# Kernel optimization log

Measured on AMD Instinct MI355X. Metric: run time of the kernel, lower is better.

Reference implementation:

```python
import jax, jax.numpy as jnp
import numpy as np
import math

B, N, D, H, FFN = 4, 2048, 512, 8, 2048
DK = D // H
EPS = 1e-5


def _layer_norm(x, g, b):
    mu = jnp.mean(x, axis=-1, keepdims=True)
    var = jnp.mean((x - mu) ** 2, axis=-1, keepdims=True)
    return (x - mu) * jax.lax.rsqrt(var + EPS) * g + b


def _rotate_half(x):
    h = x.shape[-1] // 2
    return jnp.concatenate([-x[..., h:], x[..., :h]], axis=-1)


def _rope(q, k, positions):
    # q, k: (B, H, N, DK); positions: (B, N) int
    inv_freq = 1.0 / (10000.0 ** (jnp.arange(0, DK, 2, dtype=jnp.float32) / DK))  # (DK/2,)
    ang = positions[:, None, :, None].astype(jnp.float32) * inv_freq  # (B,1,N,DK/2)
    cos = jnp.concatenate([jnp.cos(ang), jnp.cos(ang)], axis=-1)  # (B,1,N,DK)
    sin = jnp.concatenate([jnp.sin(ang), jnp.sin(ang)], axis=-1)
    q = q * cos + _rotate_half(q) * sin
    k = k * cos + _rotate_half(k) * sin
    return q, k


def setup_inputs() -> dict:
    key = jax.random.key(0)
    ks = jax.random.split(key, 16)
    s = 0.02
    x = jax.random.normal(ks[0], (B, N, D), dtype=jnp.float32)
    # backward-looking hop mask within jobs: random boolean with True diagonal
    m = jax.random.uniform(ks[1], (B, N, N)) < 0.1
    o2o_mask = m | jnp.eye(N, dtype=bool)[None]
    positions = jax.random.randint(ks[2], (B, N), 0, N)
    params = {
        'wq': jax.random.normal(ks[3], (D, D)) * s, 'bq': jnp.zeros((D,)),
        'wk': jax.random.normal(ks[4], (D, D)) * s, 'bk': jnp.zeros((D,)),
        'wv': jax.random.normal(ks[5], (D, D)) * s, 'bv': jnp.zeros((D,)),
        'wo': jax.random.normal(ks[6], (D, D)) * s, 'bo': jnp.zeros((D,)),
        'ln1_g': jnp.ones((D,)), 'ln1_b': jnp.zeros((D,)),
        'ln2_g': jnp.ones((D,)), 'ln2_b': jnp.zeros((D,)),
        'w1': jax.random.normal(ks[7], (D, FFN)) * s, 'b1': jnp.zeros((FFN,)),
        'w2': jax.random.normal(ks[8], (FFN, D)) * s, 'b2': jnp.zeros((D,)),
    }
    return {'x': x, 'o2o_mask': o2o_mask, 'positions': positions, **params}


def reference(x, o2o_mask, positions, wq, bq, wk, bk, wv, bv, wo, bo,
              ln1_g, ln1_b, ln2_g, ln2_b, w1, b1, w2, b2):
    residual = x
    xn = _layer_norm(x, ln1_g, ln1_b)
    q = (xn @ wq + bq).reshape(B, N, H, DK).transpose(0, 2, 1, 3)
    k = (xn @ wk + bk).reshape(B, N, H, DK).transpose(0, 2, 1, 3)
    v = (xn @ wv + bv).reshape(B, N, H, DK).transpose(0, 2, 1, 3)
    q, k = _rope(q, k, positions)
    scores = jnp.einsum('bhqd,bhkd->bhqk', q, k) / math.sqrt(DK)
    scores = jnp.where(o2o_mask[:, None], scores, -jnp.inf)
    attn = jax.nn.softmax(scores, axis=-1)
    attn = jnp.where(jnp.isnan(attn), 0.0, attn)  # fully-masked rows -> 0
    attn_out = jnp.einsum('bhqk,bhkd->bhqd', attn, v)
    attn_out = attn_out.transpose(0, 2, 1, 3).reshape(B, N, D)
    x = residual + (attn_out @ wo + bo)
    residual = x
    h = _layer_norm(x, ln2_g, ln2_b)
    h = jax.nn.relu(h @ w1 + b1) @ w2 + b2
    return residual + h
```

## Files before the change

kernel.cpp:

```cpp
#include <hip/hip_runtime.h>
#include <hip/hip_bf16.h>
#include <math.h>

typedef __attribute__((ext_vector_type(8))) __bf16 bf16x8;
typedef __attribute__((ext_vector_type(4))) __bf16 bf16x4;
typedef __attribute__((ext_vector_type(4))) float f32x4;

#define B_ 4
#define N_ 2048
#define D_ 512
#define H_ 8
#define DK_ 64
#define F_ 2048

__device__ __forceinline__ void async16(const __bf16* g, __bf16* l) {
  __builtin_amdgcn_global_load_lds((const __attribute__((address_space(1))) void*)g,
                                   (__attribute__((address_space(3))) void*)l, 16, 0, 0);
}

__global__ __launch_bounds__(256) void prep_all(const float* __restrict__ wq,
                                                const float* __restrict__ wk,
                                                const float* __restrict__ wv,
                                                const float* __restrict__ wo,
                                                const float* __restrict__ w1,
                                                const float* __restrict__ w2,
                                                const float* __restrict__ bq,
                                                const float* __restrict__ bk,
                                                const float* __restrict__ bv,
                                                __bf16* __restrict__ wqkvt,
                                                __bf16* __restrict__ wot,
                                                __bf16* __restrict__ w1t,
                                                __bf16* __restrict__ w2t,
                                                float* __restrict__ bqkv) {
  const int id = blockIdx.x;
  if (id >= 768) {
    int i = (id - 768) * 256 + threadIdx.x;
    bqkv[i] = (i < 512) ? bq[i] : (i < 1024) ? bk[i - 512] : bv[i - 1024];
    return;
  }
  __shared__ float t[64][65];
  const float* in;
  __bf16* outp;
  int k0, n0, K, Nc;
  if (id < 256) {
    const float* src[4] = {wq, wk, wv, wo};
    __bf16* dst[4] = {wqkvt, wqkvt + 512 * 512, wqkvt + 1024 * 512, wot};
    int w = id >> 6, tl = id & 63;
    in = src[w]; outp = dst[w]; k0 = (tl & 7) * 64; n0 = (tl >> 3) * 64; K = 512; Nc = 512;
  } else if (id < 512) {
    int tl = id - 256;
    in = w1; outp = w1t; k0 = (tl & 7) * 64; n0 = (tl >> 3) * 64; K = 512; Nc = 2048;
  } else {
    int tl = id - 512;
    in = w2; outp = w2t; k0 = (tl & 31) * 64; n0 = (tl >> 5) * 64; K = 2048; Nc = 512;
  }
  const int c = threadIdx.x & 63, r4 = threadIdx.x >> 6;
#pragma unroll
  for (int p = 0; p < 16; p++) {
    int rr = p * 4 + r4;
    t[rr][c] = in[(size_t)(k0 + rr) * Nc + n0 + c];
  }
  __syncthreads();
#pragma unroll
  for (int p = 0; p < 16; p++) {
    int rr = p * 4 + r4;
    outp[(size_t)(n0 + rr) * K + k0 + c] = (__bf16)t[c][rr];
  }
}

__global__ __launch_bounds__(256) void build_bitmask(const int* __restrict__ mask,
                                                     unsigned long long* __restrict__ bm) {
  size_t t = (size_t)blockIdx.x * 256 + threadIdx.x;
  int m = mask[t];
  unsigned long long w = __ballot(m != 0);
  if ((threadIdx.x & 63) == 0) bm[t >> 6] = w;
}

__global__ __launch_bounds__(256) void ln_fwd(const float* __restrict__ x,
                                              const float* __restrict__ g,
                                              const float* __restrict__ b,
                                              __bf16* __restrict__ out) {
  int row = blockIdx.x * 4 + (threadIdx.x >> 6);
  int lane = threadIdx.x & 63;
  const float* xr = x + (size_t)row * D_ + lane * 8;
  float4 a0 = *(const float4*)xr;
  float4 a1 = *(const float4*)(xr + 4);
  float v[8] = {a0.x, a0.y, a0.z, a0.w, a1.x, a1.y, a1.z, a1.w};
  float s = 0.f;
#pragma unroll
  for (int i = 0; i < 8; i++) s += v[i];
#pragma unroll
  for (int off = 1; off < 64; off <<= 1) s += __shfl_xor(s, off);
  float mu = s * (1.f / D_);
  float q = 0.f;
#pragma unroll
  for (int i = 0; i < 8; i++) { float d = v[i] - mu; q += d * d; }
#pragma unroll
  for (int off = 1; off < 64; off <<= 1) q += __shfl_xor(q, off);
  float rs = rsqrtf(q * (1.f / D_) + 1e-5f);
  const float* gp = g + lane * 8;
  const float* bp = b + lane * 8;
  alignas(16) __bf16 o[8];
#pragma unroll
  for (int i = 0; i < 8; i++) o[i] = (__bf16)((v[i] - mu) * rs * gp[i] + bp[i]);
  *(bf16x8*)(out + (size_t)row * D_ + lane * 8) = *(bf16x8*)o;
}

__global__ __launch_bounds__(256) void rope_vtrans(const __bf16* __restrict__ qkv,
                                                   const int* __restrict__ pos,
                                                   __bf16* __restrict__ qo,
                                                   __bf16* __restrict__ ko,
                                                   __bf16* __restrict__ vt) {
  __shared__ __bf16 tl[64][65];
  const int id = blockIdx.x;
  if (id < 8192) {
    int t = id * 256 + threadIdx.x;
    int d = t & 31;
    int h = (t >> 5) & 7;
    int n = (t >> 8) & (N_ - 1);
    int b = t >> 19;
    const __bf16* base = qkv + (size_t)(b * N_ + n) * 1536 + h * 64 + d;
    float q1 = (float)base[0], q2 = (float)base[32];
    float k1 = (float)base[512], k2 = (float)base[544];
    float p = (float)pos[b * N_ + n];
    float inv = __expf(-(float)d * (9.210340371976184f / 32.f));
    float ang = p * inv;
    float sn, cs;
    sincosf(ang, &sn, &cs);
    const float SC = 0.125f;
    size_t ob = ((size_t)(b * H_ + h) * N_ + n) * DK_ + d;
    qo[ob]      = (__bf16)((q1 * cs - q2 * sn) * SC);
    qo[ob + 32] = (__bf16)((q2 * cs + q1 * sn) * SC);
    ko[ob]      = (__bf16)(k1 * cs - k2 * sn);
    ko[ob + 32] = (__bf16)(k2 * cs + k1 * sn);
  } else {
    const int lin = id - 8192;
    const int n0 = (lin & 31) * 64, h = (lin >> 5) & 7, b = lin >> 8;
    const int c = threadIdx.x & 63, rr = threadIdx.x >> 6;
#pragma unroll
    for (int p = 0; p < 16; p++) {
      int i = p * 4 + rr;
      tl[i][c] = qkv[(size_t)(b * N_ + n0 + i) * 1536 + 1024 + h * 64 + c];
    }
    __syncthreads();
    size_t ob = (size_t)(b * H_ + h) * DK_ * N_;
#pragma unroll
    for (int p = 0; p < 16; p++) {
      int dd = p * 4 + rr;
      vt[ob + (size_t)dd * N_ + n0 + c] = tl[c][dd];
    }
  }
}

template <int RELU, int OBF, int RES>
__global__ __launch_bounds__(256) void gemm_bt(const __bf16* __restrict__ A,
                                               const __bf16* __restrict__ Bt,
                                               const float* __restrict__ bias,
                                               const float* __restrict__ res,
                                               void* __restrict__ Cout,
                                               int M, int N, int K) {
  __shared__ __bf16 As[2][128 * 32];
  __shared__ __bf16 Bs[2][128 * 32];
  const int tid = threadIdx.x;
  const int lane = tid & 63;
  const int wave = tid >> 6;
  const int quad = lane >> 4;
  const int l16 = lane & 15;
  const int m0 = blockIdx.y * 128;
  const int n0 = blockIdx.x * 128;
  const int wm = (wave >> 1) * 64;
  const int wn = (wave & 1) * 64;
  f32x4 acc[4][4] = {};

  const int c0 = tid, c1 = tid + 256;
  const int ar0 = c0 >> 2, ak0 = (c0 & 3) * 8;
  const int ar1 = c1 >> 2, ak1 = (c1 & 3) * 8;

  auto stage = [&](int k0, int buf) {
    async16(A + (size_t)(m0 + ar0) * K + k0 + ak0, As[buf] + c0 * 8);
    async16(A + (size_t)(m0 + ar1) * K + k0 + ak1, As[buf] + c1 * 8);
    async16(Bt + (size_t)(n0 + ar0) * K + k0 + ak0, Bs[buf] + c0 * 8);
    async16(Bt + (size_t)(n0 + ar1) * K + k0 + ak1, Bs[buf] + c1 * 8);
  };

  stage(0, 0);
  __syncthreads();
  const int niter = K >> 5;
  for (int it = 0; it < niter; it++) {
    const int buf = it & 1;
    if (it + 1 < niter) stage((it + 1) * 32, buf ^ 1);
    bf16x8 af[4], bf[4];
#pragma unroll
    for (int mi = 0; mi < 4; mi++)
      af[mi] = *(const bf16x8*)(As[buf] + (wm + mi * 16 + l16) * 32 + quad * 8);
#pragma unroll
    for (int ni = 0; ni < 4; ni++)
      bf[ni] = *(const bf16x8*)(Bs[buf] + (wn + ni * 16 + l16) * 32 + quad * 8);
#pragma unroll
    for (int mi = 0; mi < 4; mi++)
#pragma unroll
      for (int ni = 0; ni < 4; ni++)
        acc[mi][ni] = __builtin_amdgcn_mfma_f32_16x16x32_bf16(af[mi], bf[ni], acc[mi][ni], 0, 0, 0);
    __syncthreads();
  }
#pragma unroll
  for (int ni = 0; ni < 4; ni++) {
    const int col = n0 + wn + ni * 16 + l16;
    const float bv = bias[col];
#pragma unroll
    for (int mi = 0; mi < 4; mi++) {
#pragma unroll
      for (int r = 0; r < 4; r++) {
        const int row = m0 + wm + mi * 16 + quad * 4 + r;
        float v = acc[mi][ni][r] + bv;
        if (RES) v += res[(size_t)row * N + col];
        if (RELU) v = fmaxf(v, 0.f);
        if (OBF) ((__bf16*)Cout)[(size_t)row * N + col] = (__bf16)v;
        else     ((float*)Cout)[(size_t)row * N + col] = v;
      }
    }
  }
}

template <int RELU, int OBF, int RES>
__global__ __launch_bounds__(256) void gemm_bt64(const __bf16* __restrict__ A,
                                                 const __bf16* __restrict__ Bt,
                                                 const float* __restrict__ bias,
                                                 const float* __restrict__ res,
                                                 void* __restrict__ Cout,
                                                 int M, int N, int K) {
  __shared__ __bf16 As[2][128 * 32];
  __shared__ __bf16 Bs[2][64 * 32];
  const int tid = threadIdx.x;
  const int lane = tid & 63;
  const int wave = tid >> 6;
  const int quad = lane >> 4;
  const int l16 = lane & 15;
  const int m0 = blockIdx.y * 128;
  const int n0 = blockIdx.x * 64;
  const int wm = wave * 32;
  f32x4 acc[2][4] = {};

  const int ar0 = tid >> 2, ak0 = (tid & 3) * 8;

  auto stage = [&](int k0, int buf) {
    async16(A + (size_t)(m0 + ar0) * K + k0 + ak0, As[buf] + tid * 8);
    async16(A + (size_t)(m0 + 64 + ar0) * K + k0 + ak0, As[buf] + (tid + 256) * 8);
    async16(Bt + (size_t)(n0 + ar0) * K + k0 + ak0, Bs[buf] + tid * 8);
  };

  stage(0, 0);
  __syncthreads();
  const int niter = K >> 5;
  for (int it = 0; it < niter; it++) {
    const int buf = it & 1;
    if (it + 1 < niter) stage((it + 1) * 32, buf ^ 1);
    bf16x8 af[2], bf[4];
#pragma unroll
    for (int mi = 0; mi < 2; mi++)
      af[mi] = *(const bf16x8*)(As[buf] + (wm + mi * 16 + l16) * 32 + quad * 8);
#pragma unroll
    for (int ni = 0; ni < 4; ni++)
      bf[ni] = *(const bf16x8*)(Bs[buf] + (ni * 16 + l16) * 32 + quad * 8);
#pragma unroll
    for (int mi = 0; mi < 2; mi++)
#pragma unroll
      for (int ni = 0; ni < 4; ni++)
        acc[mi][ni] = __builtin_amdgcn_mfma_f32_16x16x32_bf16(af[mi], bf[ni], acc[mi][ni], 0, 0, 0);
    __syncthreads();
  }
#pragma unroll
  for (int ni = 0; ni < 4; ni++) {
    const int col = n0 + ni * 16 + l16;
    const float bv = bias[col];
#pragma unroll
    for (int mi = 0; mi < 2; mi++) {
#pragma unroll
      for (int r = 0; r < 4; r++) {
        const int row = m0 + wm + mi * 16 + quad * 4 + r;
        float v = acc[mi][ni][r] + bv;
        if (RES) v += res[(size_t)row * N + col];
        if (RELU) v = fmaxf(v, 0.f);
        if (OBF) ((__bf16*)Cout)[(size_t)row * N + col] = (__bf16)v;
        else     ((float*)Cout)[(size_t)row * N + col] = v;
      }
    }
  }
}

__global__ __launch_bounds__(512, 4) void flash_attn(const __bf16* __restrict__ q,
                                                     const __bf16* __restrict__ k,
                                                     const __bf16* __restrict__ vt,
                                                     const unsigned long long* __restrict__ bm,
                                                     __bf16* __restrict__ out) {
  const int bid = blockIdx.x;
  const int gl = ((bid & 7) << 6) | (bid >> 3);
  const int qt = gl & 15;
  const int h = (gl >> 4) & 7;
  const int b = gl >> 7;
  const int tid = threadIdx.x;
  const int lane = tid & 63, wave = tid >> 6;
  const int quad = lane >> 4, l16 = lane & 15;
  __shared__ __bf16 Ks[3][64 * 64];
  __shared__ __bf16 Vs[3][64 * 64];
  __shared__ __bf16 P[8][16 * 68];
  const size_t bh = (size_t)b * H_ + h;
  const __bf16* qp = q + (bh * N_ + qt * 128 + wave * 16) * DK_;
  bf16x8 qf[2];
#pragma unroll
  for (int ks = 0; ks < 2; ks++)
    qf[ks] = *(const bf16x8*)(qp + l16 * DK_ + ks * 32 + quad * 8);
  const __bf16* kbase = k + bh * N_ * DK_;
  const __bf16* vbase = vt + bh * DK_ * N_;
  const int qrow0 = qt * 128 + wave * 16 + l16;
  const unsigned long long* bmr = bm + (size_t)(b * N_ + qrow0) * (N_ / 64);
  const int xo = l16 & 7;

  f32x4 oacc[4] = {};
  float lsum = 0.f;

  const int sr = tid >> 3;
  const int sj = (tid & 7) ^ (sr & 7);
  const __bf16* ksrc = kbase + sr * DK_ + sj * 8;
  const __bf16* vsrc = vbase + (size_t)sr * N_ + sj * 8;

  auto stage = [&](int kt, int buf) {
    async16(ksrc + (size_t)kt * 64 * DK_, Ks[buf] + tid * 8);
    async16(vsrc + kt * 64, Vs[buf] + tid * 8);
  };

  stage(0, 0);
  stage(1, 1);
  unsigned long long mw = bmr[0];
  asm volatile("s_waitcnt vmcnt(3)" ::: "memory");
  __builtin_amdgcn_s_barrier();
  __builtin_amdgcn_sched_barrier(0);

  for (int kt = 0; kt < 32; kt++) {
    const int buf = kt % 3;
    const int nstage = (kt + 2 < 32) ? kt + 2 : 31;
    stage(nstage, (kt + 2) % 3);
    const int nmask = (kt + 1 < 32) ? kt + 1 : 31;
    const unsigned long long mw_nxt = bmr[nmask];

    const unsigned long long mws = mw >> (quad * 4);
#pragma unroll
    for (int ci = 0; ci < 4; ci++) {
      const int row = ci * 16 + l16;
      bf16x8 kf0 = *(const bf16x8*)(Ks[buf] + (row * 8 + (quad ^ xo)) * 8);
      bf16x8 kf1 = *(const bf16x8*)(Ks[buf] + (row * 8 + ((4 + quad) ^ xo)) * 8);
      f32x4 a = {0.f, 0.f, 0.f, 0.f};
      a = __builtin_amdgcn_mfma_f32_16x16x32_bf16(kf0, qf[0], a, 0, 0, 0);
      a = __builtin_amdgcn_mfma_f32_16x16x32_bf16(kf1, qf[1], a, 0, 0, 0);
      const unsigned int nib = (unsigned int)(mws >> (ci * 16)) & 15u;
      bf16x4 pk;
#pragma unroll
      for (int r4 = 0; r4 < 4; r4++) {
        float in = ((nib >> r4) & 1u) ? a[r4] : -1e30f;
        float p = __expf(in);
        lsum += p;
        pk[r4] = (__bf16)p;
      }
      *(bf16x4*)(&P[wave][0] + l16 * 68 + ci * 16 + quad * 4) = pk;
    }
    bf16x8 pf0 = *(const bf16x8*)(&P[wave][0] + l16 * 68 + quad * 8);
    bf16x8 pf1 = *(const bf16x8*)(&P[wave][0] + l16 * 68 + 32 + quad * 8);
#pragma unroll
    for (int ni = 0; ni < 4; ni++) {
      const int row = ni * 16 + l16;
      bf16x8 vf0 = *(const bf16x8*)(Vs[buf] + (row * 8 + (quad ^ xo)) * 8);
      bf16x8 vf1 = *(const bf16x8*)(Vs[buf] + (row * 8 + ((4 + quad) ^ xo)) * 8);
      oacc[ni] = __builtin_amdgcn_mfma_f32_16x16x32_bf16(vf0, pf0, oacc[ni], 0, 0, 0);
      oacc[ni] = __builtin_amdgcn_mfma_f32_16x16x32_bf16(vf1, pf1, oacc[ni], 0, 0, 0);
    }
    asm volatile("s_waitcnt vmcnt(3)" ::: "memory");
    __builtin_amdgcn_s_barrier();
    __builtin_amdgcn_sched_barrier(0);
    mw = mw_nxt;
  }
  lsum += __shfl_xor(lsum, 16);
  lsum += __shfl_xor(lsum, 32);
  const float inv_l = (lsum > 0.f) ? 1.f / lsum : 0.f;
#pragma unroll
  for (int ni = 0; ni < 4; ni++) {
    bf16x4 ov;
#pragma unroll
    for (int r = 0; r < 4; r++) ov[r] = (__bf16)(oacc[ni][r] * inv_l);
    *(bf16x4*)(out + ((size_t)b * N_ + qrow0) * D_ + h * DK_ + ni * 16 + quad * 4) = ov;
  }
}

static constexpr size_t OFF_XN  = 0;
static constexpr size_t OFF_WT  = 8388608;
static constexpr size_t OFF_WO  = OFF_WT + 1572864;
static constexpr size_t OFF_W1  = OFF_WO + 524288;
static constexpr size_t OFF_W2  = OFF_W1 + 2097152;
static constexpr size_t OFF_BQ  = OFF_W2 + 2097152;
static constexpr size_t OFF_QKV = OFF_BQ + 6144;
static constexpr size_t OFF_QR  = OFF_QKV + 25165824;
static constexpr size_t OFF_KR  = OFF_QR + 8388608;
static constexpr size_t OFF_VT  = OFF_KR + 8388608;
static constexpr size_t OFF_AO  = OFF_VT + 8388608;
static constexpr size_t OFF_Y   = OFF_AO + 8388608;

extern "C" void kernel_launch(void* const* d_in, const int* in_sizes, int n_in,
                              void* d_out, int out_size, void* d_ws, size_t ws_size,
                              hipStream_t stream) {
  const float* x    = (const float*)d_in[0];
  const int*   mask = (const int*)d_in[1];
  const int*   pos  = (const int*)d_in[2];
  const float* wq   = (const float*)d_in[3];
  const float* bq   = (const float*)d_in[4];
  const float* wk   = (const float*)d_in[5];
  const float* bk   = (const float*)d_in[6];
  const float* wv   = (const float*)d_in[7];
  const float* bv   = (const float*)d_in[8];
  const float* wo   = (const float*)d_in[9];
  const float* bo   = (const float*)d_in[10];
  const float* ln1g = (const float*)d_in[11];
  const float* ln1b = (const float*)d_in[12];
  const float* ln2g = (const float*)d_in[13];
  const float* ln2b = (const float*)d_in[14];
  const float* w1   = (const float*)d_in[15];
  const float* b1   = (const float*)d_in[16];
  const float* w2   = (const float*)d_in[17];
  const float* b2   = (const float*)d_in[18];
  float* out = (float*)d_out;
  char* ws = (char*)d_ws;

  __bf16* xn    = (__bf16*)(ws + OFF_XN);
  __bf16* wqkvt = (__bf16*)(ws + OFF_WT);
  __bf16* wot   = (__bf16*)(ws + OFF_WO);
  __bf16* w1t   = (__bf16*)(ws + OFF_W1);
  __bf16* w2t   = (__bf16*)(ws + OFF_W2);
  float*  bqkv  = (float*)(ws + OFF_BQ);
  __bf16* qkv   = (__bf16*)(ws + OFF_QKV);
  __bf16* qr    = (__bf16*)(ws + OFF_QR);
  __bf16* kr    = (__bf16*)(ws + OFF_KR);
  __bf16* vt    = (__bf16*)(ws + OFF_VT);
  __bf16* attn  = (__bf16*)(ws + OFF_AO);
  float*  y     = (float*)(ws + OFF_Y);
  unsigned long long* bm = (unsigned long long*)(ws + OFF_Y);
  __bf16* hn    = xn;
  __bf16* h2    = qkv;

  dim3 b256(256);
  dim3 b512(512);
  prep_all<<<774, b256, 0, stream>>>(wq, wk, wv, wo, w1, w2, bq, bk, bv,
                                     wqkvt, wot, w1t, w2t, bqkv);
  build_bitmask<<<65536, b256, 0, stream>>>(mask, bm);
  ln_fwd<<<2048, b256, 0, stream>>>(x, ln1g, ln1b, xn);
  gemm_bt<0, 1, 0><<<dim3(12, 64), b256, 0, stream>>>(xn, wqkvt, bqkv, nullptr, qkv, 8192, 1536, 512);
  rope_vtrans<<<9216, b256, 0, stream>>>(qkv, pos, qr, kr, vt);
  flash_attn<<<512, b512, 0, stream>>>(qr, kr, vt, bm, attn);
  gemm_bt64<0, 0, 1><<<dim3(8, 64), b256, 0, stream>>>(attn, wot, bo, x, y, 8192, 512, 512);
  ln_fwd<<<2048, b256, 0, stream>>>(y, ln2g, ln2b, hn);
  gemm_bt<1, 1, 0><<<dim3(16, 64), b256, 0, stream>>>(hn, w1t, b1, nullptr, h2, 8192, 2048, 512);
  gemm_bt64<0, 0, 1><<<dim3(8, 64), b256, 0, stream>>>(h2, w2t, b2, y, out, 8192, 512, 2048);
}
```

Before: 362.8 us.

## Software-pipeline attention loop: overlap next tile's QK softmax with current PV

```diff
diff --git a/kernel.cpp b/kernel.cpp
--- a/kernel.cpp
+++ b/kernel.cpp
@@ -329,26 +329,15 @@
     async16(vsrc + kt * 64, Vs[buf] + tid * 8);
   };
 
-  stage(0, 0);
-  stage(1, 1);
-  unsigned long long mw = bmr[0];
-  asm volatile("s_waitcnt vmcnt(3)" ::: "memory");
-  __builtin_amdgcn_s_barrier();
-  __builtin_amdgcn_sched_barrier(0);
-
-  for (int kt = 0; kt < 32; kt++) {
-    const int buf = kt % 3;
-    const int nstage = (kt + 2 < 32) ? kt + 2 : 31;
-    stage(nstage, (kt + 2) % 3);
-    const int nmask = (kt + 1 < 32) ? kt + 1 : 31;
-    const unsigned long long mw_nxt = bmr[nmask];
-
-    const unsigned long long mws = mw >> (quad * 4);
+  __bf16* Pw = &P[wave][0] + l16 * 68;
+
+  auto qk_softmax = [&](const __bf16* KT, unsigned long long mwv, bf16x8& po0, bf16x8& po1) {
+    const unsigned long long mws = mwv >> (quad * 4);
 #pragma unroll
     for (int ci = 0; ci < 4; ci++) {
       const int row = ci * 16 + l16;
-      bf16x8 kf0 = *(const bf16x8*)(Ks[buf] + (row * 8 + (quad ^ xo)) * 8);
-      bf16x8 kf1 = *(const bf16x8*)(Ks[buf] + (row * 8 + ((4 + quad) ^ xo)) * 8);
+      bf16x8 kf0 = *(const bf16x8*)(KT + (row * 8 + (quad ^ xo)) * 8);
+      bf16x8 kf1 = *(const bf16x8*)(KT + (row * 8 + ((4 + quad) ^ xo)) * 8);
       f32x4 a = {0.f, 0.f, 0.f, 0.f};
       a = __builtin_amdgcn_mfma_f32_16x16x32_bf16(kf0, qf[0], a, 0, 0, 0);
       a = __builtin_amdgcn_mfma_f32_16x16x32_bf16(kf1, qf[1], a, 0, 0, 0);
@@ -361,23 +350,51 @@
         lsum += p;
         pk[r4] = (__bf16)p;
       }
-      *(bf16x4*)(&P[wave][0] + l16 * 68 + ci * 16 + quad * 4) = pk;
-    }
-    bf16x8 pf0 = *(const bf16x8*)(&P[wave][0] + l16 * 68 + quad * 8);
-    bf16x8 pf1 = *(const bf16x8*)(&P[wave][0] + l16 * 68 + 32 + quad * 8);
+      *(bf16x4*)(Pw + ci * 16 + quad * 4) = pk;
+    }
+    po0 = *(const bf16x8*)(Pw + quad * 8);
+    po1 = *(const bf16x8*)(Pw + 32 + quad * 8);
+  };
+
+  auto pv = [&](const __bf16* VT, bf16x8 p0, bf16x8 p1) {
 #pragma unroll
     for (int ni = 0; ni < 4; ni++) {
       const int row = ni * 16 + l16;
-      bf16x8 vf0 = *(const bf16x8*)(Vs[buf] + (row * 8 + (quad ^ xo)) * 8);
-      bf16x8 vf1 = *(const bf16x8*)(Vs[buf] + (row * 8 + ((4 + quad) ^ xo)) * 8);
-      oacc[ni] = __builtin_amdgcn_mfma_f32_16x16x32_bf16(vf0, pf0, oacc[ni], 0, 0, 0);
-      oacc[ni] = __builtin_amdgcn_mfma_f32_16x16x32_bf16(vf1, pf1, oacc[ni], 0, 0, 0);
-    }
-    asm volatile("s_waitcnt vmcnt(3)" ::: "memory");
+      bf16x8 vf0 = *(const bf16x8*)(VT + (row * 8 + (quad ^ xo)) * 8);
+      bf16x8 vf1 = *(const bf16x8*)(VT + (row * 8 + ((4 + quad) ^ xo)) * 8);
+      oacc[ni] = __builtin_amdgcn_mfma_f32_16x16x32_bf16(vf0, p0, oacc[ni], 0, 0, 0);
+      oacc[ni] = __builtin_amdgcn_mfma_f32_16x16x32_bf16(vf1, p1, oacc[ni], 0, 0, 0);
+    }
+  };
+
+  stage(0, 0);
+  stage(1, 1);
+  asm volatile("s_waitcnt vmcnt(2)" ::: "memory");
+  __builtin_amdgcn_s_barrier();
+  __builtin_amdgcn_sched_barrier(0);
+  unsigned long long m0 = bmr[0];
+  unsigned long long mcur = bmr[1];
+  bf16x8 pc0, pc1;
+  qk_softmax(Ks[0], m0, pc0, pc1);
+  asm volatile("s_waitcnt vmcnt(0)" ::: "memory");
+  __builtin_amdgcn_s_barrier();
+  __builtin_amdgcn_sched_barrier(0);
+
+  for (int kt = 0; kt < 31; kt++) {
+    const int ns = (kt + 2 < 32) ? kt + 2 : 31;
+    stage(ns, (kt + 2) % 3);
+    __builtin_amdgcn_sched_barrier(0);
+    const unsigned long long mfut = bmr[ns];
+    bf16x8 pn0, pn1;
+    qk_softmax(Ks[(kt + 1) % 3], mcur, pn0, pn1);
+    pv(Vs[kt % 3], pc0, pc1);
+    asm volatile("s_waitcnt vmcnt(1)" ::: "memory");
     __builtin_amdgcn_s_barrier();
     __builtin_amdgcn_sched_barrier(0);
-    mw = mw_nxt;
-  }
+    pc0 = pn0; pc1 = pn1; mcur = mfut;
+  }
+  pv(Vs[31 % 3], pc0, pc1);
+
   lsum += __shfl_xor(lsum, 16);
   lsum += __shfl_xor(lsum, 32);
   const float inv_l = (lsum > 0.f) ? 1.f / lsum : 0.f;
```

After: 374.0 us. +3.1%, slower.
